# Kernel optimization log

Hardware: AMD Instinct MI355X
Metric: run time of the kernel (lower is better)

The kernel has to match this reference:

```python
import jax, jax.numpy as jnp
import numpy as np

B, T, IN = 128, 2048, 32      # batch, seq_len, input dim
S, M = 32, 8                  # kaarma state dim, number of ensemble models
E, H = 64, 128                # encoder dim, controller GRU hidden
CIN = E + 1                   # controller input = [encoded, error]


def setup_inputs() -> dict:
    key = jax.random.key(0)
    ks = jax.random.split(key, 15)
    sc = 0.1  # small init scale keeps tanh/sigmoid in sane range
    return {
        "x": jax.random.normal(ks[0], (B, T, IN), jnp.float32),
        "y": jax.random.normal(ks[1], (B, T), jnp.float32),
        # mkaarma params: shared encoder + per-model recurrent state update
        "W_enc": jax.random.normal(ks[2], (IN, E), jnp.float32) * sc,
        "b_enc": jnp.zeros((E,), jnp.float32),
        "W_in": jax.random.normal(ks[3], (M, IN, S), jnp.float32) * sc,
        "W_rec": jax.random.normal(ks[4], (M, S, S), jnp.float32) * sc,
        "b_s": jnp.zeros((M, S), jnp.float32),
        # controller params: GRU cell + gate head
        "W_x": jax.random.normal(ks[5], (CIN, 3 * H), jnp.float32) * sc,
        "W_h": jax.random.normal(ks[6], (H, 3 * H), jnp.float32) * sc,
        "b_x": jnp.zeros((3 * H,), jnp.float32),
        "b_h": jnp.zeros((3 * H,), jnp.float32),
        "W_gate": jax.random.normal(ks[7], (H, M), jnp.float32) * sc,
        "b_gate": jnp.zeros((M,), jnp.float32),
    }


def reference(x, y, W_enc, b_enc, W_in, W_rec, b_s,
              W_x, W_h, b_x, b_h, W_gate, b_gate):
    Bv = x.shape[0]
    dt = x.dtype

    def step(carry, xy):
        kstate, h, err = carry            # [B,S], [B,H], [B]
        x_t, y_t = xy                     # [B,IN], [B]
        # mkaarma: encode input + ensemble of candidate next states
        encoded = jnp.tanh(x_t @ W_enc + b_enc)                        # [B,E]
        new_state = jnp.tanh(
            jnp.einsum('bi,mis->bms', x_t, W_in)
            + jnp.einsum('bs,msd->bmd', kstate, W_rec)
            + b_s
        )                                                              # [B,M,S]
        # controller: GRU cell on [encoded, error]
        inp = jnp.concatenate([encoded, err[:, None]], axis=1)         # [B,E+1]
        xz, xr, xn = jnp.split(inp @ W_x + b_x, 3, axis=1)
        hz, hr, hn = jnp.split(h @ W_h + b_h, 3, axis=1)
        z = jax.nn.sigmoid(xz + hz)
        r = jax.nn.sigmoid(xr + hr)
        n = jnp.tanh(xn + r * hn)
        h_new = (1.0 - z) * n + z * h                                  # [B,H]
        # gate softmax over models, mix candidate states
        gate = jax.nn.softmax(h_new @ W_gate + b_gate, axis=1)         # [B,M]
        kstate_new = jnp.einsum('bm,bms->bs', gate, new_state)         # [B,S]
        pred = kstate_new[:, -1]                                       # [B]
        err_new = pred - y_t
        return (kstate_new, h_new, err_new), pred

    init = (jnp.zeros((Bv, S), dt), jnp.zeros((Bv, H), dt), jnp.zeros((Bv,), dt))
    xs = (jnp.swapaxes(x, 0, 1), jnp.swapaxes(y, 0, 1))   # time-major
    _, preds = jax.lax.scan(step, init, xs)               # [T,B]
    return jnp.swapaxes(preds, 0, 1)                      # [B,T]
```

## Files before the change

kernel.cpp:

```cpp
#include <hip/hip_runtime.h>

typedef _Float16 h2 __attribute__((ext_vector_type(2)));
typedef _Float16 h8 __attribute__((ext_vector_type(8)));

#define NB 128
#define NT 2048
#define NIN 32
#define NS 32
#define NM 8
#define NE 64
#define NH 128
#define NH3 384

__device__ __forceinline__ h2 mkh2(float a, float b) {
  h2 r; r[0] = (_Float16)a; r[1] = (_Float16)b; return r;
}

template <int I>
__device__ __forceinline__ h2 pick2(h8 v) {
  return __builtin_shufflevector(v, v, 2 * I, 2 * I + 1);
}

__device__ __forceinline__ float fdot2(h2 a, h2 b, float c) {
#if __has_builtin(__builtin_amdgcn_fdot2)
  return __builtin_amdgcn_fdot2(a, b, c, false);
#else
  return c + (float)a[0] * (float)b[0] + (float)a[1] * (float)b[1];
#endif
}

__device__ __forceinline__ float rcpf(float v) {
#if __has_builtin(__builtin_amdgcn_rcpf)
  return __builtin_amdgcn_rcpf(v);
#else
  return 1.0f / v;
#endif
}

__device__ __forceinline__ float sigmoid_f(float v) { return rcpf(1.0f + __expf(-v)); }
__device__ __forceinline__ float tanh_f(float v) { return 1.0f - 2.0f * rcpf(1.0f + __expf(2.0f * v)); }

template <int CTRL>
__device__ __forceinline__ float dppadd(float v) {
  int t = __builtin_amdgcn_update_dpp(0, __float_as_int(v), CTRL, 0xF, 0xF, true);
  return v + __int_as_float(t);
}
__device__ __forceinline__ float wave_reduce63(float v) {
  v = dppadd<0x111>(v); v = dppadd<0x112>(v); v = dppadd<0x114>(v);
  v = dppadd<0x118>(v); v = dppadd<0x142>(v); v = dppadd<0x143>(v);
  return v;
}
__device__ __forceinline__ float pairsum(float v) {
  int t = __builtin_amdgcn_update_dpp(0, __float_as_int(v), 0xB1, 0xF, 0xF, true);
  return v + __int_as_float(t);
}

__device__ __forceinline__ void lds_fence() {
  asm volatile("s_waitcnt lgkmcnt(0)" ::: "memory");
}

#define RPW 16
__global__ __launch_bounds__(256, 1) void pre2(
    const float* __restrict__ gx, const float* __restrict__ W_enc,
    const float* __restrict__ b_enc, const float* __restrict__ W_x,
    const float* __restrict__ b_x, _Float16* __restrict__ xpre,
    _Float16* __restrict__ xh16, int t0, int CH) {
  const int tid = threadIdx.x, wv = tid >> 6, lane = tid & 63;
  __shared__ __align__(16) _Float16 x16[4][NIN];
  __shared__ __align__(16) _Float16 encA[4][RPW][NE];

  h2 we[16];
#pragma unroll
  for (int i = 0; i < 16; ++i)
    we[i] = mkh2(W_enc[(2 * i) * NE + lane], W_enc[(2 * i + 1) * NE + lane]);
  const float be = b_enc[lane];

  const int g0 = ((int)blockIdx.x * 4 + wv) * RPW;

  h2 wx3[96];
#pragma unroll 1
  for (int pass = 0; pass < 2; ++pass) {
#pragma unroll
    for (int kk = 0; kk < 3; ++kk) {
      const int j = lane + 64 * (3 * pass + kk);
#pragma unroll
      for (int i = 0; i < 32; ++i)
        wx3[kk * 32 + i] = mkh2(W_x[(size_t)(2 * i) * NH3 + j], W_x[(size_t)(2 * i + 1) * NH3 + j]);
    }
#pragma unroll 1
    for (int r = 0; r < RPW; ++r) {
      const int g = g0 + r;
      const int bb = g / CH, tc = g % CH;
      if (pass == 0) {
        const float* xr = gx + ((size_t)bb * NT + t0 + tc) * NIN;
        if (lane < NIN) x16[wv][lane] = (_Float16)xr[lane];
        lds_fence();
        if (lane < 16) {
          const unsigned v = *(const unsigned*)&x16[wv][2 * lane];
          ((unsigned*)xh16)[(size_t)g * 16 + lane] = v;
        }
        const h8* xv8 = (const h8*)x16[wv];
        float a = be;
#pragma unroll
        for (int i = 0; i < 4; ++i) {
          const h8 xv = xv8[i];
          a = fdot2(pick2<0>(xv), we[4 * i + 0], a);
          a = fdot2(pick2<1>(xv), we[4 * i + 1], a);
          a = fdot2(pick2<2>(xv), we[4 * i + 2], a);
          a = fdot2(pick2<3>(xv), we[4 * i + 3], a);
        }
        encA[wv][r][lane] = (_Float16)tanh_f(a);
        lds_fence();
      }
      const h8* ev8 = (const h8*)encA[wv][r];
      h8 ev[8];
#pragma unroll
      for (int i = 0; i < 8; ++i) ev[i] = ev8[i];
#pragma unroll
      for (int kk = 0; kk < 3; ++kk) {
        const int j = lane + 64 * (3 * pass + kk);
        float a = b_x[j], c = 0.f;
#pragma unroll
        for (int i = 0; i < 8; ++i) {
          a = fdot2(pick2<0>(ev[i]), wx3[kk * 32 + 4 * i + 0], a);
          c = fdot2(pick2<1>(ev[i]), wx3[kk * 32 + 4 * i + 1], c);
          a = fdot2(pick2<2>(ev[i]), wx3[kk * 32 + 4 * i + 2], a);
          c = fdot2(pick2<3>(ev[i]), wx3[kk * 32 + 4 * i + 3], c);
        }
        xpre[(size_t)g * NH3 + j] = (_Float16)(a + c);
      }
    }
  }
}

__global__ __launch_bounds__(384, 2) void rnn7(
    const float* __restrict__ gy, const _Float16* __restrict__ xpre,
    const _Float16* __restrict__ xh16,
    const float* __restrict__ W_h, const float* __restrict__ b_h,
    const float* __restrict__ W_in, const float* __restrict__ W_rec,
    const float* __restrict__ b_s, const float* __restrict__ W_x,
    const float* __restrict__ W_gate, const float* __restrict__ b_gate,
    float* __restrict__ out, float* __restrict__ state, int t0, int CH) {
  const int tid = threadIdx.x;
  const int b = blockIdx.x;
  const int wv = tid >> 6;
  const int lane = tid & 63;

  __shared__ __align__(16) _Float16 h_sh[2][NH];
  __shared__ __align__(16) _Float16 xpre_sh[2][NH3];
  __shared__ __align__(16) float ns_sh[2][NS][NM];
  __shared__ __align__(16) float xd_sh[2][2 * NH];
  __shared__ __align__(16) float gp_sh[2][4][NM];
  __shared__ __align__(16) _Float16 kst_sh[NS];
  __shared__ float err_sh;
  __shared__ float y_lds[NT];

  float* st = state + b * (NH + NS + 1);

  h2 wbig[96];
  h2 wrec[16];
  float wg[8];
  float bh[3], wxe[3];
  float bs4[4];
  float bg[8];
  float h_prev = 0.f;
  unsigned xpq[12];
  h8 xr0[4], xr1[4], xr2[4], xr3[4];

  const int gl = tid - 128;
  const int j = gl >> 1;
  const int half = gl & 1;

  for (int i = tid; i < CH; i += 384) y_lds[i] = gy[(size_t)b * NT + t0 + i];

  if (wv >= 2) {
#pragma unroll
    for (int g = 0; g < 3; ++g) {
      const int jc = j + 128 * g;
#pragma unroll
      for (int i = 0; i < 32; ++i)
        wbig[g * 32 + i] = mkh2(W_h[(size_t)(64 * half + 2 * i) * NH3 + jc],
                                W_h[(size_t)(64 * half + 2 * i + 1) * NH3 + jc]);
      bh[g] = b_h[jc];
      wxe[g] = W_x[(size_t)NE * NH3 + jc];
    }
#pragma unroll
    for (int m = 0; m < 8; ++m) wg[m] = half ? 0.f : W_gate[j * NM + m];
    {
      const int m0 = gl >> 5, d0 = gl & 31;
#pragma unroll
      for (int i = 0; i < 16; ++i)
        wrec[i] = mkh2(W_rec[m0 * 1024 + (2 * i) * 32 + d0],
                       W_rec[m0 * 1024 + (2 * i + 1) * 32 + d0]);
    }
    h_prev = t0 ? st[j] : 0.f;
    if (!half) h_sh[1][j] = (_Float16)h_prev;
  } else if (wv == 1) {
#pragma unroll
    for (int k = 0; k < 4; ++k) {
      const int o = lane + 64 * k, m = o >> 5, d = o & 31;
#pragma unroll
      for (int i = 0; i < 16; ++i)
        wbig[k * 16 + i] = mkh2(W_in[m * 1024 + (2 * i) * 32 + d],
                                W_in[m * 1024 + (2 * i + 1) * 32 + d]);
      bs4[k] = b_s[o];
    }
    {
      const h8* x0 = (const h8*)(xh16 + (size_t)(b * CH) * NIN);
#pragma unroll
      for (int i = 0; i < 4; ++i) xr0[i] = x0[i];
#pragma unroll
      for (int k = 0; k < 4; ++k) {
        float s = bs4[k];
#pragma unroll
        for (int i = 0; i < 4; ++i) {
          s = fdot2(pick2<0>(xr0[i]), wbig[k * 16 + 4 * i + 0], s);
          s = fdot2(pick2<1>(xr0[i]), wbig[k * 16 + 4 * i + 1], s);
          s = fdot2(pick2<2>(xr0[i]), wbig[k * 16 + 4 * i + 2], s);
          s = fdot2(pick2<3>(xr0[i]), wbig[k * 16 + 4 * i + 3], s);
        }
        xd_sh[1][lane + 64 * k] = s;
      }
    }
  } else {
#pragma unroll
    for (int m = 0; m < 8; ++m) bg[m] = b_gate[m];
    if (lane < NS) kst_sh[lane] = t0 ? (_Float16)st[NH + lane] : (_Float16)0.f;
    if (lane == 0) err_sh = t0 ? st[NH + NS] : 0.f;
  }
  __syncthreads();

  float hz = 0.f, hr = 0.f, hn = 0.f;

#define STEPK(K, XRK)                                                          \
  {                                                                            \
    const int tc = tc4 + (K);                                                  \
    const int q = (K) & 1, qp = q ^ 1;                                         \
                                 \
    if (wv >= 2) {                                                             \
      const h8* hv8 = (const h8*)&h_sh[qp][64 * half];                         \
      float a0 = 0.f, c0 = 0.f, a1 = 0.f, c1 = 0.f, a2 = 0.f, c2 = 0.f;        \
      _Pragma("unroll")                                                        \
      for (int i = 0; i < 8; ++i) {                                            \
        const h8 hv = hv8[i];                                                  \
        a0 = fdot2(pick2<0>(hv), wbig[4 * i + 0], a0);                         \
        c0 = fdot2(pick2<1>(hv), wbig[4 * i + 1], c0);                         \
        a0 = fdot2(pick2<2>(hv), wbig[4 * i + 2], a0);                         \
        c0 = fdot2(pick2<3>(hv), wbig[4 * i + 3], c0);                         \
        a1 = fdot2(pick2<0>(hv), wbig[32 + 4 * i + 0], a1);                    \
        c1 = fdot2(pick2<1>(hv), wbig[32 + 4 * i + 1], c1);                    \
        a1 = fdot2(pick2<2>(hv), wbig[32 + 4 * i + 2], a1);                    \
        c1 = fdot2(pick2<3>(hv), wbig[32 + 4 * i + 3], c1);                    \
        a2 = fdot2(pick2<0>(hv), wbig[64 + 4 * i + 0], a2);                    \
        c2 = fdot2(pick2<1>(hv), wbig[64 + 4 * i + 1], c2);                    \
        a2 = fdot2(pick2<2>(hv), wbig[64 + 4 * i + 2], a2);                    \
        c2 = fdot2(pick2<3>(hv), wbig[64 + 4 * i + 3], c2);                    \
      }                                                                        \
      hz = pairsum(a0 + c0) + bh[0];                                           \
      hr = pairsum(a1 + c1) + bh[1];                                           \
      hn = pairsum(a2 + c2) + bh[2];                                           \
    } else if (wv == 0) {                                                      \
      if (tc > 0) {                                                            \
        const int u = lane & 31;                                               \
        const float4* nsv = (const float4*)&ns_sh[qp][u][0];                   \
        const float4 n0 = nsv[0], n1 = nsv[1];                                 \
        const float4* g4 = (const float4*)&gp_sh[qp][0][0];                    \
        float4 A = g4[0], Bv = g4[1];                                          \
        A.x += g4[2].x + g4[4].x + g4[6].x; A.y += g4[2].y + g4[4].y + g4[6].y;\
        A.z += g4[2].z + g4[4].z + g4[6].z; A.w += g4[2].w + g4[4].w + g4[6].w;\
        Bv.x += g4[3].x + g4[5].x + g4[7].x; Bv.y += g4[3].y + g4[5].y + g4[7].y;\
        Bv.z += g4[3].z + g4[5].z + g4[7].z; Bv.w += g4[3].w + g4[5].w + g4[7].w;\
        float l[8] = {A.x + bg[0], A.y + bg[1], A.z + bg[2], A.w + bg[3],      \
                      Bv.x + bg[4], Bv.y + bg[5], Bv.z + bg[6], Bv.w + bg[7]}; \
        float mx = fmaxf(fmaxf(fmaxf(l[0], l[1]), fmaxf(l[2], l[3])),          \
                         fmaxf(fmaxf(l[4], l[5]), fmaxf(l[6], l[7])));         \
        float e[8], s = 0.f;                                                   \
        _Pragma("unroll")                                                      \
        for (int m = 0; m < 8; ++m) { e[m] = __expf(l[m] - mx); s += e[m]; }   \
        float ks = e[0] * n0.x + e[1] * n0.y + e[2] * n0.z + e[3] * n0.w +     \
                   e[4] * n1.x + e[5] * n1.y + e[6] * n1.z + e[7] * n1.w;      \
        ks *= rcpf(s);                                                         \
        if (lane < NS) kst_sh[u] = (_Float16)ks;                               \
        if (lane == 31) {                                                      \
          out[(size_t)b * NT + t0 + tc - 1] = ks;                              \
          err_sh = ks - y_lds[tc - 1];                                         \
        }                                                                      \
      }                                                                        \
    } else {    \
      if ((K) == 0) {                                                          \
        const unsigned* xpg = (const unsigned*)xpre;                           \
        _Pragma("unroll")                                                      \
        for (int k = 0; k < 4; ++k) {                                          \
          const size_t rr = (size_t)(b * CH + tc4 + k) * 192;                  \
          xpq[3 * k + 0] = xpg[rr + lane];                                     \
          xpq[3 * k + 1] = xpg[rr + lane + 64];                                \
          xpq[3 * k + 2] = xpg[rr + lane + 128];                               \
        }                                                                      \
        const h8* xg0 = (const h8*)(xh16 + (size_t)(b * CH + min(tc4 + 1, CH - 1)) * NIN); \
        const h8* xg1 = (const h8*)(xh16 + (size_t)(b * CH + min(tc4 + 2, CH - 1)) * NIN); \
        const h8* xg2 = (const h8*)(xh16 + (size_t)(b * CH + min(tc4 + 3, CH - 1)) * NIN); \
        const h8* xg3 = (const h8*)(xh16 + (size_t)(b * CH + min(tc4 + 4, CH - 1)) * NIN); \
        _Pragma("unroll")                                                      \
        for (int i = 0; i < 4; ++i) {                                          \
          xr0[i] = xg0[i]; xr1[i] = xg1[i]; xr2[i] = xg2[i]; xr3[i] = xg3[i];  \
        }                                                                      \
      }                                                                        \
      unsigned* xps = (unsigned*)&xpre_sh[q][0];                               \
      xps[lane] = xpq[3 * (K) + 0];                                            \
      xps[lane + 64] = xpq[3 * (K) + 1];                                       \
      xps[lane + 128] = xpq[3 * (K) + 2];                                      \
    }                                                                          \
    __syncthreads();                                                           \
                                 \
    if (wv >= 2) {                                                             \
      const float err = err_sh;                                                \
      const float xz = (float)xpre_sh[q][j] + err * wxe[0];                    \
      const float xr = (float)xpre_sh[q][j + 128] + err * wxe[1];              \
      const float xn = (float)xpre_sh[q][j + 256] + err * wxe[2];              \
      const float z = sigmoid_f(hz + xz);                                      \
      const float r = sigmoid_f(hr + xr);                                      \
      const float n = tanh_f(xn + r * hn);                                     \
      const float hnew = (1.f - z) * n + z * h_prev;                           \
      h_prev = hnew;                                                           \
      if (!half) h_sh[q][j] = (_Float16)hnew;                                  \
      float p[8];                                                              \
      _Pragma("unroll")                                                        \
      for (int m = 0; m < 8; ++m) p[m] = wave_reduce63(hnew * wg[m]);          \
      if (lane == 63) {                                                        \
        *(float4*)&gp_sh[q][wv - 2][0] = make_float4(p[0], p[1], p[2], p[3]);  \
        *(float4*)&gp_sh[q][wv - 2][4] = make_float4(p[4], p[5], p[6], p[7]);  \
      }                                                                        \
      const h8* kv8 = (const h8*)kst_sh;                                       \
      float s = xd_sh[qp][gl];                                                 \
      _Pragma("unroll")                                                        \
      for (int i = 0; i < 4; ++i) {                                            \
        const h8 kv = kv8[i];                                                  \
        s = fdot2(pick2<0>(kv), wrec[4 * i + 0], s);                           \
        s = fdot2(pick2<1>(kv), wrec[4 * i + 1], s);                           \
        s = fdot2(pick2<2>(kv), wrec[4 * i + 2], s);                           \
        s = fdot2(pick2<3>(kv), wrec[4 * i + 3], s);                           \
      }                                                                        \
      ns_sh[q][gl & 31][gl >> 5] = tanh_f(s);                                  \
    } else if (wv == 1) {                                                      \
      if (tc + 1 < CH) {                                                       \
        _Pragma("unroll")                                                      \
        for (int k = 0; k < 4; ++k) {                                          \
          float s = bs4[k];                                                    \
          _Pragma("unroll")                                                    \
          for (int i = 0; i < 4; ++i) {                                        \
            s = fdot2(pick2<0>(XRK[i]), wbig[k * 16 + 4 * i + 0], s);          \
            s = fdot2(pick2<1>(XRK[i]), wbig[k * 16 + 4 * i + 1], s);          \
            s = fdot2(pick2<2>(XRK[i]), wbig[k * 16 + 4 * i + 2], s);          \
            s = fdot2(pick2<3>(XRK[i]), wbig[k * 16 + 4 * i + 3], s);          \
          }                                                                    \
          xd_sh[q][lane + 64 * k] = s;                                         \
        }                                                                      \
      }                                                                        \
    }                                                                          \
    __syncthreads();                                                           \
  }

  for (int tc4 = 0; tc4 < CH; tc4 += 4) {
    STEPK(0, xr0)
    STEPK(1, xr1)
    STEPK(2, xr2)
    STEPK(3, xr3)
  }
#undef STEPK

  if (wv == 0) {
    const int qf = (CH - 1) & 1;
    const int u = lane & 31;
    const float4* nsv = (const float4*)&ns_sh[qf][u][0];
    const float4 n0 = nsv[0], n1 = nsv[1];
    const float4* g4 = (const float4*)&gp_sh[qf][0][0];
    float4 A = g4[0], Bv = g4[1];
    A.x += g4[2].x + g4[4].x + g4[6].x; A.y += g4[2].y + g4[4].y + g4[6].y;
    A.z += g4[2].z + g4[4].z + g4[6].z; A.w += g4[2].w + g4[4].w + g4[6].w;
    Bv.x += g4[3].x + g4[5].x + g4[7].x; Bv.y += g4[3].y + g4[5].y + g4[7].y;
    Bv.z += g4[3].z + g4[5].z + g4[7].z; Bv.w += g4[3].w + g4[5].w + g4[7].w;
    float l[8] = {A.x + bg[0], A.y + bg[1], A.z + bg[2], A.w + bg[3],
                  Bv.x + bg[4], Bv.y + bg[5], Bv.z + bg[6], Bv.w + bg[7]};
    float mx = fmaxf(fmaxf(fmaxf(l[0], l[1]), fmaxf(l[2], l[3])),
                     fmaxf(fmaxf(l[4], l[5]), fmaxf(l[6], l[7])));
    float e[8], s = 0.f;
#pragma unroll
    for (int m = 0; m < 8; ++m) { e[m] = __expf(l[m] - mx); s += e[m]; }
    float ks = e[0] * n0.x + e[1] * n0.y + e[2] * n0.z + e[3] * n0.w +
               e[4] * n1.x + e[5] * n1.y + e[6] * n1.z + e[7] * n1.w;
    ks *= rcpf(s);
    if (lane < NS) st[NH + u] = ks;
    if (lane == 31) {
      out[(size_t)b * NT + t0 + CH - 1] = ks;
      st[NH + NS] = ks - y_lds[CH - 1];
    }
  }
  if (wv >= 2 && !half) st[j] = h_prev;
}

extern "C" void kernel_launch(void* const* d_in, const int* in_sizes, int n_in,
                              void* d_out, int out_size, void* d_ws, size_t ws_size,
                              hipStream_t stream) {
  const float* x = (const float*)d_in[0];
  const float* y = (const float*)d_in[1];
  const float* W_enc = (const float*)d_in[2];
  const float* b_enc = (const float*)d_in[3];
  const float* W_in = (const float*)d_in[4];
  const float* W_rec = (const float*)d_in[5];
  const float* b_s = (const float*)d_in[6];
  const float* W_x = (const float*)d_in[7];
  const float* W_h = (const float*)d_in[8];
  const float* b_x = (const float*)d_in[9];
  const float* b_h = (const float*)d_in[10];
  const float* W_gate = (const float*)d_in[11];
  const float* b_gate = (const float*)d_in[12];
  float* out = (float*)d_out;

  const size_t stateB = (size_t)NB * (NH + NS + 1) * sizeof(float);
  int CH = NT;
  while (CH > 4) {
    const size_t need = (size_t)NB * CH * NH3 * 2 + (size_t)NB * CH * NIN * 2 + stateB;
    if (need <= ws_size) break;
    CH >>= 1;
  }

  _Float16* xpre = (_Float16*)d_ws;
  _Float16* xh16 = (_Float16*)((char*)d_ws + (size_t)NB * CH * NH3 * 2);
  float* state = (float*)((char*)d_ws + (size_t)NB * CH * NH3 * 2 + (size_t)NB * CH * NIN * 2);

  for (int t0 = 0; t0 < NT; t0 += CH) {
    pre2<<<dim3(2 * CH), dim3(256), 0, stream>>>(
        x, W_enc, b_enc, W_x, b_x, xpre, xh16, t0, CH);
    rnn7<<<dim3(NB), dim3(384), 0, stream>>>(
        y, xpre, xh16, W_h, b_h, W_in, W_rec, b_s, W_x, W_gate, b_gate,
        out, state, t0, CH);
  }
}
```

Before: 2.591 ms.

## Fuse precompute and recurrence into one launch with per-chunk ready flags

Merges the input-projection precompute kernel and the recurrent kernel into a single launch. The first NB blocks run the recurrence and extra blocks compute xpre/xh16 in 64-step chunks, each publishing an atomic flag. Recurrent blocks spin-wait on the flag for the chunk they need before loading, so the precompute overlaps with the sequential recurrence instead of fully preceding it. This relies on the recurrent blocks (lowest block indices) being resident alongside producers without deadlock. It also adds a flag memset per chunk, and launch bounds drop to one block per CU.

Result: faster. 2.525 ms (median of 2 runs) (-2.6%).

```diff
diff --git a/kernel.cpp b/kernel.cpp
--- a/kernel.cpp
+++ b/kernel.cpp
@@ -11,6 +11,7 @@
 #define NE 64
 #define NH 128
 #define NH3 384
+#define RPW 16
 
 __device__ __forceinline__ h2 mkh2(float a, float b) {
   h2 r; r[0] = (_Float16)a; r[1] = (_Float16)b; return r;
@@ -40,6 +41,12 @@
 __device__ __forceinline__ float sigmoid_f(float v) { return rcpf(1.0f + __expf(-v)); }
 __device__ __forceinline__ float tanh_f(float v) { return 1.0f - 2.0f * rcpf(1.0f + __expf(2.0f * v)); }
 
+__device__ __forceinline__ float f16bits_tof(unsigned short u) {
+  _Float16 h;
+  __builtin_memcpy(&h, &u, 2);
+  return (float)h;
+}
+
 template <int CTRL>
 __device__ __forceinline__ float dppadd(float v) {
   int t = __builtin_amdgcn_update_dpp(0, __float_as_int(v), CTRL, 0xF, 0xF, true);
@@ -59,93 +66,25 @@
   asm volatile("s_waitcnt lgkmcnt(0)" ::: "memory");
 }
 
-#define RPW 16
-__global__ __launch_bounds__(256, 1) void pre2(
-    const float* __restrict__ gx, const float* __restrict__ W_enc,
-    const float* __restrict__ b_enc, const float* __restrict__ W_x,
-    const float* __restrict__ b_x, _Float16* __restrict__ xpre,
-    _Float16* __restrict__ xh16, int t0, int CH) {
-  const int tid = threadIdx.x, wv = tid >> 6, lane = tid & 63;
+__device__ __forceinline__ void waitflag(int* f) {
+  while (__hip_atomic_load(f, __ATOMIC_ACQUIRE, __HIP_MEMORY_SCOPE_AGENT) == 0)
+    __builtin_amdgcn_s_sleep(2);
+}
+
+__global__ __launch_bounds__(384, 1) void fused(
+    const float* __restrict__ gx, const float* __restrict__ gy,
+    const float* __restrict__ W_enc, const float* __restrict__ b_enc,
+    const float* __restrict__ W_in, const float* __restrict__ W_rec,
+    const float* __restrict__ b_s, const float* __restrict__ W_x,
+    const float* __restrict__ W_h, const float* __restrict__ b_x,
+    const float* __restrict__ b_h, const float* __restrict__ W_gate,
+    const float* __restrict__ b_gate, _Float16* __restrict__ xpre,
+    _Float16* __restrict__ xh16, float* __restrict__ out,
+    float* __restrict__ state, int* __restrict__ flags, int t0, int CH) {
+  const int tid = threadIdx.x;
+
   __shared__ __align__(16) _Float16 x16[4][NIN];
   __shared__ __align__(16) _Float16 encA[4][RPW][NE];
-
-  h2 we[16];
-#pragma unroll
-  for (int i = 0; i < 16; ++i)
-    we[i] = mkh2(W_enc[(2 * i) * NE + lane], W_enc[(2 * i + 1) * NE + lane]);
-  const float be = b_enc[lane];
-
-  const int g0 = ((int)blockIdx.x * 4 + wv) * RPW;
-
-  h2 wx3[96];
-#pragma unroll 1
-  for (int pass = 0; pass < 2; ++pass) {
-#pragma unroll
-    for (int kk = 0; kk < 3; ++kk) {
-      const int j = lane + 64 * (3 * pass + kk);
-#pragma unroll
-      for (int i = 0; i < 32; ++i)
-        wx3[kk * 32 + i] = mkh2(W_x[(size_t)(2 * i) * NH3 + j], W_x[(size_t)(2 * i + 1) * NH3 + j]);
-    }
-#pragma unroll 1
-    for (int r = 0; r < RPW; ++r) {
-      const int g = g0 + r;
-      const int bb = g / CH, tc = g % CH;
-      if (pass == 0) {
-        const float* xr = gx + ((size_t)bb * NT + t0 + tc) * NIN;
-        if (lane < NIN) x16[wv][lane] = (_Float16)xr[lane];
-        lds_fence();
-        if (lane < 16) {
-          const unsigned v = *(const unsigned*)&x16[wv][2 * lane];
-          ((unsigned*)xh16)[(size_t)g * 16 + lane] = v;
-        }
-        const h8* xv8 = (const h8*)x16[wv];
-        float a = be;
-#pragma unroll
-        for (int i = 0; i < 4; ++i) {
-          const h8 xv = xv8[i];
-          a = fdot2(pick2<0>(xv), we[4 * i + 0], a);
-          a = fdot2(pick2<1>(xv), we[4 * i + 1], a);
-          a = fdot2(pick2<2>(xv), we[4 * i + 2], a);
-          a = fdot2(pick2<3>(xv), we[4 * i + 3], a);
-        }
-        encA[wv][r][lane] = (_Float16)tanh_f(a);
-        lds_fence();
-      }
-      const h8* ev8 = (const h8*)encA[wv][r];
-      h8 ev[8];
-#pragma unroll
-      for (int i = 0; i < 8; ++i) ev[i] = ev8[i];
-#pragma unroll
-      for (int kk = 0; kk < 3; ++kk) {
-        const int j = lane + 64 * (3 * pass + kk);
-        float a = b_x[j], c = 0.f;
-#pragma unroll
-        for (int i = 0; i < 8; ++i) {
-          a = fdot2(pick2<0>(ev[i]), wx3[kk * 32 + 4 * i + 0], a);
-          c = fdot2(pick2<1>(ev[i]), wx3[kk * 32 + 4 * i + 1], c);
-          a = fdot2(pick2<2>(ev[i]), wx3[kk * 32 + 4 * i + 2], a);
-          c = fdot2(pick2<3>(ev[i]), wx3[kk * 32 + 4 * i + 3], c);
-        }
-        xpre[(size_t)g * NH3 + j] = (_Float16)(a + c);
-      }
-    }
-  }
-}
-
-__global__ __launch_bounds__(384, 2) void rnn7(
-    const float* __restrict__ gy, const _Float16* __restrict__ xpre,
-    const _Float16* __restrict__ xh16,
-    const float* __restrict__ W_h, const float* __restrict__ b_h,
-    const float* __restrict__ W_in, const float* __restrict__ W_rec,
-    const float* __restrict__ b_s, const float* __restrict__ W_x,
-    const float* __restrict__ W_gate, const float* __restrict__ b_gate,
-    float* __restrict__ out, float* __restrict__ state, int t0, int CH) {
-  const int tid = threadIdx.x;
-  const int b = blockIdx.x;
-  const int wv = tid >> 6;
-  const int lane = tid & 63;
-
   __shared__ __align__(16) _Float16 h_sh[2][NH];
   __shared__ __align__(16) _Float16 xpre_sh[2][NH3];
   __shared__ __align__(16) float ns_sh[2][NS][NM];
@@ -154,6 +93,89 @@
   __shared__ __align__(16) _Float16 kst_sh[NS];
   __shared__ float err_sh;
   __shared__ float y_lds[NT];
+
+  if (blockIdx.x >= NB) {
+    const int pb = (int)blockIdx.x - NB;
+    const int bb = pb % NB;
+    const int cc = pb / NB;
+    if (tid < 256) {
+      const int wv = tid >> 6, lane = tid & 63;
+      h2 we[16];
+#pragma unroll
+      for (int i = 0; i < 16; ++i)
+        we[i] = mkh2(W_enc[(2 * i) * NE + lane], W_enc[(2 * i + 1) * NE + lane]);
+      const float be = b_enc[lane];
+      const int tc0 = cc * 64 + wv * RPW;
+
+      h2 wx3[96];
+#pragma unroll 1
+      for (int pass = 0; pass < 2; ++pass) {
+#pragma unroll
+        for (int kk = 0; kk < 3; ++kk) {
+          const int j = lane + 64 * (3 * pass + kk);
+#pragma unroll
+          for (int i = 0; i < 32; ++i)
+            wx3[kk * 32 + i] = mkh2(W_x[(size_t)(2 * i) * NH3 + j],
+                                    W_x[(size_t)(2 * i + 1) * NH3 + j]);
+        }
+#pragma unroll 1
+        for (int r = 0; r < RPW; ++r) {
+          const int tc = tc0 + r;
+          const size_t g = (size_t)bb * CH + tc;
+          if (pass == 0) {
+            const float* xr = gx + ((size_t)bb * NT + t0 + tc) * NIN;
+            if (lane < NIN) x16[wv][lane] = (_Float16)xr[lane];
+            lds_fence();
+            if (lane < 16) {
+              const unsigned v = *(const unsigned*)&x16[wv][2 * lane];
+              ((unsigned*)xh16)[g * 16 + lane] = v;
+            }
+            const h8* xv8 = (const h8*)x16[wv];
+            float a = be;
+#pragma unroll
+            for (int i = 0; i < 4; ++i) {
+              const h8 xv = xv8[i];
+              a = fdot2(pick2<0>(xv), we[4 * i + 0], a);
+              a = fdot2(pick2<1>(xv), we[4 * i + 1], a);
+              a = fdot2(pick2<2>(xv), we[4 * i + 2], a);
+              a = fdot2(pick2<3>(xv), we[4 * i + 3], a);
+            }
+            encA[wv][r][lane] = (_Float16)tanh_f(a);
+            lds_fence();
+          }
+          const h8* ev8 = (const h8*)encA[wv][r];
+          h8 ev[8];
+#pragma unroll
+          for (int i = 0; i < 8; ++i) ev[i] = ev8[i];
+#pragma unroll
+          for (int kk = 0; kk < 3; ++kk) {
+            const int j = lane + 64 * (3 * pass + kk);
+            float a = b_x[j], c = 0.f;
+#pragma unroll
+            for (int i = 0; i < 8; ++i) {
+              a = fdot2(pick2<0>(ev[i]), wx3[kk * 32 + 4 * i + 0], a);
+              c = fdot2(pick2<1>(ev[i]), wx3[kk * 32 + 4 * i + 1], c);
+              a = fdot2(pick2<2>(ev[i]), wx3[kk * 32 + 4 * i + 2], a);
+              c = fdot2(pick2<3>(ev[i]), wx3[kk * 32 + 4 * i + 3], c);
+            }
+            xpre[g * NH3 + j] = (_Float16)(a + c);
+          }
+        }
+      }
+    }
+    asm volatile("s_waitcnt vmcnt(0)" ::: "memory");
+    __syncthreads();
+    if (tid == 0) {
+      __threadfence();
+      __hip_atomic_store(&flags[pb], 1, __ATOMIC_RELEASE,
+                         __HIP_MEMORY_SCOPE_AGENT);
+    }
+    return;
+  }
+
+  const int b = blockIdx.x;
+  const int wv = tid >> 6;
+  const int lane = tid & 63;
 
   float* st = state + b * (NH + NS + 1);
 
@@ -166,6 +188,7 @@
   float h_prev = 0.f;
   unsigned xpq[12];
   h8 xr0[4], xr1[4], xr2[4], xr3[4];
+  int readyf = -1;
 
   const int gl = tid - 128;
   const int j = gl >> 1;
@@ -205,6 +228,8 @@
                                 W_in[m * 1024 + (2 * i + 1) * 32 + d]);
       bs4[k] = b_s[o];
     }
+    waitflag(&flags[b]);
+    readyf = b;
     {
       const h8* x0 = (const h8*)(xh16 + (size_t)(b * CH) * NIN);
 #pragma unroll
@@ -286,8 +311,10 @@
           err_sh = ks - y_lds[tc - 1];                                         \
         }                                                                      \
       }                                                                        \
-    } else {    \
+    } else {              \
       if ((K) == 0) {                                                          \
+        const int needf = (min(tc4 + 8, CH - 1) >> 6) * NB + b;                \
+        if (needf > readyf) { waitflag(&flags[needf]); readyf = needf; }       \
         const unsigned* xpg = (const unsigned*)xpre;                           \
         _Pragma("unroll")                                                      \
         for (int k = 0; k < 4; ++k) {                                          \
@@ -418,21 +445,24 @@
 
   const size_t stateB = (size_t)NB * (NH + NS + 1) * sizeof(float);
   int CH = NT;
-  while (CH > 4) {
-    const size_t need = (size_t)NB * CH * NH3 * 2 + (size_t)NB * CH * NIN * 2 + stateB;
+  while (CH > 64) {
+    const size_t need = (size_t)NB * CH * NH3 * 2 + (size_t)NB * CH * NIN * 2 +
+                        stateB + (size_t)(NB * CH / 64) * sizeof(int);
     if (need <= ws_size) break;
     CH >>= 1;
   }
+  const int npre = NB * CH / 64;
 
   _Float16* xpre = (_Float16*)d_ws;
   _Float16* xh16 = (_Float16*)((char*)d_ws + (size_t)NB * CH * NH3 * 2);
-  float* state = (float*)((char*)d_ws + (size_t)NB * CH * NH3 * 2 + (size_t)NB * CH * NIN * 2);
+  float* state = (float*)((char*)d_ws + (size_t)NB * CH * NH3 * 2 +
+                          (size_t)NB * CH * NIN * 2);
+  int* flags = (int*)((char*)state + stateB);
 
   for (int t0 = 0; t0 < NT; t0 += CH) {
-    pre2<<<dim3(2 * CH), dim3(256), 0, stream>>>(
-        x, W_enc, b_enc, W_x, b_x, xpre, xh16, t0, CH);
-    rnn7<<<dim3(NB), dim3(384), 0, stream>>>(
-        y, xpre, xh16, W_h, b_h, W_in, W_rec, b_s, W_x, W_gate, b_gate,
-        out, state, t0, CH);
-  }
-}
+    (void)hipMemsetAsync(flags, 0, (size_t)npre * sizeof(int), stream);
+    fused<<<dim3(NB + npre), dim3(384), 0, stream>>>(
+        x, y, W_enc, b_enc, W_in, W_rec, b_s, W_x, W_h, b_x, b_h, W_gate,
+        b_gate, xpre, xh16, out, state, flags, t0, CH);
+  }
+}
```
